# Optimization experiments

Hardware: AMD Instinct MI355X
Metric: run time of the kernel (lower is better)

Reference implementation:

```python
import jax, jax.numpy as jnp
import numpy as np

D_MODEL = 1024
N_HEADS = 16
D_HEAD = 64
B, S = 2, 2048


def setup_inputs() -> dict:
    key = jax.random.key(0)
    ks = jax.random.split(key, 16)
    HDH = N_HEADS * D_HEAD
    s = 0.02
    return {
        "h": jax.random.normal(ks[0], (B, S, D_MODEL), dtype=jnp.float32),
        "att_mask": jax.random.randint(ks[1], (B, S), 0, 2) > 0,
        "Wq": jax.random.normal(ks[2], (D_MODEL, HDH), dtype=jnp.float32) * s,
        "bq": jnp.zeros((HDH,), dtype=jnp.float32),
        "Wkv": jax.random.normal(ks[3], (D_MODEL, 2 * HDH), dtype=jnp.float32) * s,
        "bkv": jnp.zeros((2 * HDH,), dtype=jnp.float32),
        "Wo": jax.random.normal(ks[4], (HDH, D_MODEL), dtype=jnp.float32) * s,
        "bo": jnp.zeros((D_MODEL,), dtype=jnp.float32),
        "W1": jax.random.normal(ks[5], (D_MODEL, D_MODEL), dtype=jnp.float32) * s,
        "b1": jnp.zeros((D_MODEL,), dtype=jnp.float32),
        "W2": jax.random.normal(ks[6], (D_MODEL, D_MODEL), dtype=jnp.float32) * s,
        "b2": jnp.zeros((D_MODEL,), dtype=jnp.float32),
        "ln_g": jnp.ones((D_MODEL,), dtype=jnp.float32),
        "ln_b": jnp.zeros((D_MODEL,), dtype=jnp.float32),
    }


def _layer_norm(x, g, b, eps=1e-6):
    mu = jnp.mean(x, axis=-1, keepdims=True)
    var = jnp.mean(jnp.square(x - mu), axis=-1, keepdims=True)
    return (x - mu) * jax.lax.rsqrt(var + eps) * g + b


def reference(h, att_mask, Wq, bq, Wkv, bkv, Wo, bo, W1, b1, W2, b2, ln_g, ln_b):
    bz, ln, _ = h.shape
    scale = 1.0 / (D_HEAD ** 0.5)
    q = (h @ Wq + bq).reshape(bz, ln, N_HEADS, D_HEAD)
    kv = h @ Wkv + bkv
    k, v = jnp.split(kv, 2, axis=-1)
    k = k.reshape(bz, ln, N_HEADS, D_HEAD)
    v = v.reshape(bz, ln, N_HEADS, D_HEAD)
    # scores: [b, heads, len_q, len_k]
    scores = jnp.einsum('bqhd,bkhd->bhqk', q, k) * scale
    scores = jnp.where(att_mask[:, None, None, :], -1e9, scores)
    probs = jax.nn.softmax(scores, axis=-1)
    att = jnp.einsum('bhqk,bkhd->bqhd', probs, v).reshape(bz, ln, N_HEADS * D_HEAD)
    att_out = att @ Wo + bo
    # glu_type == 1
    g = jax.nn.sigmoid(h @ W1 + b1) * (h @ W2 + b2)
    return _layer_norm(h + att_out + g, ln_g, ln_b)
```

## Files before the change

### kernel.cpp

```cpp
#include <hip/hip_runtime.h>
#include <hip/hip_bf16.h>


typedef short bf16x8 __attribute__((ext_vector_type(8)));
typedef float f32x4  __attribute__((ext_vector_type(4)));
typedef float f32x16 __attribute__((ext_vector_type(16)));
typedef unsigned int u32x4 __attribute__((ext_vector_type(4)));

typedef const __attribute__((address_space(1))) void* gas_cvp;
typedef __attribute__((address_space(3))) void* las_vp;

__device__ __forceinline__ void gload_lds16(const void* g, void* l) {
  __builtin_amdgcn_global_load_lds((gas_cvp)g, (las_vp)l, 16, 0, 0);
}

__device__ __forceinline__ short f2bf(float f) {
  __hip_bfloat16 h = __float2bfloat16(f);
  return *reinterpret_cast<short*>(&h);
}
__device__ __forceinline__ float bf2f(short s) {
  unsigned u = ((unsigned)(unsigned short)s) << 16;
  return __builtin_bit_cast(float, u);
}

#if __has_builtin(__builtin_amdgcn_exp2f)
#define EXP2(x) __builtin_amdgcn_exp2f(x)
#else
#define EXP2(x) exp2f(x)
#endif

constexpr int BATCH = 2;
constexpr int SEQ   = 2048;
constexpr int NH    = 16;
constexpr int MROWS = BATCH * SEQ;
constexpr int NSPLIT = 4;
constexpr int KSPL   = SEQ / NSPLIT;
constexpr int RH     = MROWS * NH;


__global__ __launch_bounds__(256) void cvt_bf16(const float* __restrict__ src,
                                                short* __restrict__ dst, int n4) {
  int i = blockIdx.x * 256 + threadIdx.x;
  if (i >= n4) return;
  float4 v = reinterpret_cast<const float4*>(src)[i];
  short4 o;
  o.x = f2bf(v.x); o.y = f2bf(v.y); o.z = f2bf(v.z); o.w = f2bf(v.w);
  reinterpret_cast<short4*>(dst)[i] = o;
}

struct WtA {
  const float* s[6];
  short* d[6];
  int st[6];
};
__global__ __launch_bounds__(256) void wtrans6(WtA a) {
  __shared__ float tile[32][33];
  const float* __restrict__ src = a.s[blockIdx.z];
  short* __restrict__ dst = a.d[blockIdx.z];
  const int stride = a.st[blockIdx.z];
  const int tx = threadIdx.x & 31, ty = threadIdx.x >> 5;
  const int n0 = blockIdx.x * 32, k0 = blockIdx.y * 32;
  #pragma unroll
  for (int i = 0; i < 32; i += 8)
    tile[ty + i][tx] = src[(size_t)(k0 + ty + i) * stride + n0 + tx];
  __syncthreads();
  #pragma unroll
  for (int i = 0; i < 32; i += 8)
    dst[(size_t)(n0 + ty + i) * 1024 + k0 + tx] = f2bf(tile[tx][ty + i]);
}

__global__ __launch_bounds__(256) void vtrans(const short* __restrict__ qkv,
                                              short* __restrict__ vt) {
  __shared__ short tile[32][33];
  const int tx = threadIdx.x & 31, ty = threadIdx.x >> 5;
  const int s0 = blockIdx.x * 32, d0 = blockIdx.y * 32, b = blockIdx.z;
  #pragma unroll
  for (int i = 0; i < 32; i += 8)
    tile[ty + i][tx] = qkv[(size_t)(b * SEQ + s0 + ty + i) * 3072 + 2048 + d0 + tx];
  __syncthreads();
  #pragma unroll
  for (int i = 0; i < 32; i += 8)
    vt[(size_t)(b * 1024 + d0 + ty + i) * SEQ + s0 + tx] = tile[tx][ty + i];
}

__global__ void pack_bias(const float* __restrict__ bq, const float* __restrict__ bkv,
                          const float* __restrict__ b1, const float* __restrict__ b2,
                          float* __restrict__ bqkv, float* __restrict__ b12) {
  int i = blockIdx.x * 256 + threadIdx.x;
  if (i < 1024) bqkv[i] = bq[i];
  else if (i < 3072) bqkv[i] = bkv[i - 1024];
  else if (i < 4096) b12[i - 3072] = b1[i - 3072];
  else if (i < 5120) b12[i - 3072] = b2[i - 4096];
}

__device__ __forceinline__ bool mask_at(const void* mp, int idx, int flag) {
  if (flag == 1) return ((const int*)mp)[idx] != 0;
  if (flag == 2) return ((const float*)mp)[idx] != 0.f;
  return ((const unsigned char*)mp)[idx] != 0;
}

__global__ __launch_bounds__(256) void premask(const void* __restrict__ msk,
                                               float* __restrict__ mbL) {
  __shared__ int si, sf;
  const unsigned* m = (const unsigned*)msk;
  if (threadIdx.x == 0) { si = 1; sf = 1; }
  __syncthreads();
  bool oki = true, okf = true;
  for (int i = threadIdx.x; i < 1024; i += 256) {
    unsigned v = m[i];
    oki = oki && (v <= 1u);
    okf = okf && (v == 0u || v == 0x3F800000u);
  }
  if (!oki) si = 0;
  if (!okf) sf = 0;
  __syncthreads();
  const int flag = si ? 1 : (sf ? 2 : 0);
  int i = blockIdx.x * 256 + threadIdx.x;
  if (i < MROWS) mbL[i] = mask_at(msk, i, flag) ? -1.442695e9f : -8.0f;
}

__global__ __launch_bounds__(256) void gemm_kernel(const short* __restrict__ A,
                                                   const short* __restrict__ BT,
                                                   const float* __restrict__ bias,
                                                   short* __restrict__ outp, int N) {
  __shared__ short Alds[4096];
  __shared__ short Blds[4096];
  const int tid = threadIdx.x;
  const int w = tid >> 6, lane = tid & 63, g = lane >> 4, lr = lane & 15;
  const int wr = w >> 1, wc = w & 1;
  const int bm = blockIdx.y, bn = blockIdx.x;

  f32x4 acc[4][4] = {};

  const int srow = tid >> 2;
  const int scol = (tid & 3) * 8;
  const short* Ab = A  + (size_t)(bm * 128 + srow) * 1024 + scol;
  const short* Bb = BT + (size_t)(bn * 128 + srow) * 1024 + scol;

  for (int kt = 0; kt < 32; ++kt) {
    const int kb = kt * 32;
    __syncthreads();
    gload_lds16(Ab + kb,             &Alds[tid * 8]);
    gload_lds16(Ab + 64 * 1024 + kb, &Alds[2048 + tid * 8]);
    gload_lds16(Bb + kb,             &Blds[tid * 8]);
    gload_lds16(Bb + 64 * 1024 + kb, &Blds[2048 + tid * 8]);
    asm volatile("s_waitcnt vmcnt(0)" ::: "memory");
    __syncthreads();

    bf16x8 af[4], bfr[4];
    #pragma unroll
    for (int m = 0; m < 4; ++m)
      af[m] = *reinterpret_cast<const bf16x8*>(&Alds[(wr * 64 + m * 16 + lr) * 32 + g * 8]);
    #pragma unroll
    for (int n = 0; n < 4; ++n)
      bfr[n] = *reinterpret_cast<const bf16x8*>(&Blds[(wc * 64 + n * 16 + lr) * 32 + g * 8]);
    #pragma unroll
    for (int m = 0; m < 4; ++m)
      #pragma unroll
      for (int n = 0; n < 4; ++n)
        acc[m][n] = __builtin_amdgcn_mfma_f32_16x16x32_bf16(af[m], bfr[n], acc[m][n], 0, 0, 0);
  }

  #pragma unroll
  for (int m = 0; m < 4; ++m) {
    const int row = bm * 128 + wr * 64 + m * 16 + g * 4;
    #pragma unroll
    for (int n = 0; n < 4; ++n) {
      const int col = bn * 128 + wc * 64 + n * 16 + lr;
      const float bv = bias[col];
      #pragma unroll
      for (int r = 0; r < 4; ++r)
        outp[(size_t)(row + r) * N + col] = f2bf(acc[m][n][r] + bv);
    }
  }
}

__global__ __launch_bounds__(256) void glu_kernel(const short* __restrict__ x12,
                                                  short* __restrict__ g) {
  const int i = blockIdx.x * 256 + threadIdx.x;
  const int row = i >> 7, c8 = (i & 127) * 8;
  const size_t base = (size_t)row * 2048 + c8;
  bf16x8 a = *reinterpret_cast<const bf16x8*>(&x12[base]);
  bf16x8 b = *reinterpret_cast<const bf16x8*>(&x12[base + 1024]);
  bf16x8 r;
  #pragma unroll
  for (int j = 0; j < 8; ++j) {
    const float x = bf2f(a[j]);
    r[j] = f2bf(bf2f(b[j]) / (1.f + __expf(-x)));
  }
  *reinterpret_cast<bf16x8*>(&g[(size_t)row * 1024 + c8]) = r;
}

constexpr int KB = 64;

__global__ __launch_bounds__(256) void attn_kernel(const short* __restrict__ qkv,
                                                   const short* __restrict__ vt,
                                                   const float* __restrict__ mbL,
                                                   short* __restrict__ opart,
                                                   float* __restrict__ spart) {
  __shared__ short Kl[2][64][64];
  __shared__ short Vl[2][64][64];
  __shared__ float mb[KSPL];

  const int tid = threadIdx.x;
  const int w = tid >> 6, lane = tid & 63, ql = lane & 31, hi = lane >> 5;
  const int sp = blockIdx.x & (NSPLIT - 1), qb = blockIdx.x / NSPLIT;
  const int h = blockIdx.y, b = blockIdx.z;
  const int qrow = qb * 128 + w * 32 + ql;
  const int kofs = sp * KSPL;

  bf16x8 qf[4];
  {
    const short* qp = qkv + (size_t)(b * SEQ + qrow) * 3072 + h * 64;
    #pragma unroll
    for (int c = 0; c < 4; ++c)
      qf[c] = *reinterpret_cast<const bf16x8*>(qp + c * 16 + hi * 8);
  }

  const int srow = tid >> 3, sg = tid & 7;
  auto stageKV = [&](int buf, int kt) {
    #pragma unroll
    for (int r = 0; r < 2; ++r) {
      const int row = r * 32 + srow;
      const int gsw = (sg ^ (row & 7)) * 8;
      const short* gk = qkv + (size_t)(b * SEQ + kofs + kt * KB + row) * 3072 + 1024 + h * 64 + gsw;
      gload_lds16(gk, &Kl[buf][0][0] + (r * 256 + tid) * 8);
      const short* gv = vt + (size_t)(b * 1024 + h * 64 + row) * SEQ + kofs + kt * KB + gsw;
      gload_lds16(gv, &Vl[buf][0][0] + (r * 256 + tid) * 8);
    }
  };

  float s_run = 0.f;
  f32x16 oacc0 = {}, oacc1 = {};

  if (tid < 128) gload_lds16(mbL + b * SEQ + kofs + tid * 4, &mb[tid * 4]);
  stageKV(0, 0);
  asm volatile("s_waitcnt vmcnt(0)" ::: "memory");
  __syncthreads();

  constexpr int NT = KSPL / KB;
  for (int kt = 0; kt < NT; ++kt) {
    const int cur = kt & 1;
    if (kt + 1 < NT) stageKV(cur ^ 1, kt + 1);
    const short* Kb = &Kl[cur][0][0];
    const short* Vb = &Vl[cur][0][0];

    #pragma unroll
    for (int t2 = 0; t2 < 2; ++t2) {
      const int krow = t2 * 32 + ql;
      f32x16 sc = {};
      __builtin_amdgcn_s_setprio(1);
      #pragma unroll
      for (int c = 0; c < 4; ++c) {
        bf16x8 kf = *reinterpret_cast<const bf16x8*>(
            Kb + krow * 64 + ((2 * c + hi) ^ (krow & 7)) * 8);
        sc = __builtin_amdgcn_mfma_f32_32x32x16_bf16(kf, qf[c], sc, 0, 0, 0);
      }
      __builtin_amdgcn_s_setprio(0);
      float p[16];
      #pragma unroll
      for (int u = 0; u < 4; ++u) {
        float4 m4 = *reinterpret_cast<const float4*>(&mb[kt * KB + t2 * 32 + u * 8 + hi * 4]);
        p[4 * u + 0] = EXP2(fmaf(sc[4 * u + 0], 0.18033688f, m4.x));
        p[4 * u + 1] = EXP2(fmaf(sc[4 * u + 1], 0.18033688f, m4.y));
        p[4 * u + 2] = EXP2(fmaf(sc[4 * u + 2], 0.18033688f, m4.z));
        p[4 * u + 3] = EXP2(fmaf(sc[4 * u + 3], 0.18033688f, m4.w));
      }
      {
        float a0 = (p[0] + p[1]) + (p[2] + p[3]);
        float a1 = (p[4] + p[5]) + (p[6] + p[7]);
        float a2 = (p[8] + p[9]) + (p[10] + p[11]);
        float a3 = (p[12] + p[13]) + (p[14] + p[15]);
        s_run += (a0 + a1) + (a2 + a3);
      }
      unsigned P[8];
      #pragma unroll
      for (int j = 0; j < 8; ++j)
        asm("v_cvt_pk_bf16_f32 %0, %1, %2" : "=v"(P[j]) : "v"(p[2 * j]), "v"(p[2 * j + 1]));
      asm("v_permlane32_swap_b32 %0, %1" : "+v"(P[0]), "+v"(P[2]));
      asm("v_permlane32_swap_b32 %0, %1" : "+v"(P[1]), "+v"(P[3]));
      asm("v_permlane32_swap_b32 %0, %1" : "+v"(P[4]), "+v"(P[6]));
      asm("v_permlane32_swap_b32 %0, %1" : "+v"(P[5]), "+v"(P[7]));
      u32x4 c0 = { P[0], P[1], P[2], P[3] };
      u32x4 c1 = { P[4], P[5], P[6], P[7] };
      bf16x8 pf[2] = { __builtin_bit_cast(bf16x8, c0), __builtin_bit_cast(bf16x8, c1) };

      __builtin_amdgcn_s_setprio(1);
      #pragma unroll
      for (int ch = 0; ch < 2; ++ch) {
        const int gk = t2 * 4 + ch * 2 + hi;
        bf16x8 v0 = *reinterpret_cast<const bf16x8*>(
            Vb + ql * 64 + (gk ^ (ql & 7)) * 8);
        bf16x8 v1 = *reinterpret_cast<const bf16x8*>(
            Vb + (32 + ql) * 64 + (gk ^ (ql & 7)) * 8);
        oacc0 = __builtin_amdgcn_mfma_f32_32x32x16_bf16(v0, pf[ch], oacc0, 0, 0, 0);
        oacc1 = __builtin_amdgcn_mfma_f32_32x32x16_bf16(v1, pf[ch], oacc1, 0, 0, 0);
      }
      __builtin_amdgcn_s_setprio(0);
    }
    asm volatile("s_waitcnt vmcnt(0)" ::: "memory");
    __syncthreads();
  }

  const float sT = s_run + __shfl_xor(s_run, 32);
  const size_t obase = (size_t)sp * RH * 64 + (size_t)(b * SEQ + qrow) * 1024 + h * 64;
  #pragma unroll
  for (int dt = 0; dt < 2; ++dt) {
    #pragma unroll
    for (int u = 0; u < 4; ++u) {
      short4 st;
      const f32x16& oa = dt ? oacc1 : oacc0;
      st.x = f2bf(oa[4 * u + 0]);
      st.y = f2bf(oa[4 * u + 1]);
      st.z = f2bf(oa[4 * u + 2]);
      st.w = f2bf(oa[4 * u + 3]);
      *reinterpret_cast<short4*>(&opart[obase + dt * 32 + u * 8 + hi * 4]) = st;
    }
  }
  if (hi == 0)
    spart[sp * RH + (b * SEQ + qrow) * NH + h] = sT;
}

__global__ __launch_bounds__(256) void attn_merge(const short* __restrict__ opart,
                                                  const float* __restrict__ spart,
                                                  short* __restrict__ att) {
  const int idx = blockIdx.x * 256 + threadIdx.x;
  const int rh = idx >> 3;
  const size_t base = (size_t)rh * 64 + (idx & 7) * 8;
  float acc[8] = {};
  float ss = 0.f;
  #pragma unroll
  for (int s = 0; s < NSPLIT; ++s) {
    bf16x8 o = *reinterpret_cast<const bf16x8*>(&opart[(size_t)s * RH * 64 + base]);
    #pragma unroll
    for (int j = 0; j < 8; ++j) acc[j] += bf2f(o[j]);
    ss += spart[s * RH + rh];
  }
  const float inv = 1.f / ss;
  bf16x8 r;
  #pragma unroll
  for (int j = 0; j < 8; ++j) r[j] = f2bf(acc[j] * inv);
  *reinterpret_cast<bf16x8*>(&att[base]) = r;
}

__global__ __launch_bounds__(256) void ln_kernel(const float* __restrict__ h,
                                                 const short* __restrict__ ao,
                                                 const short* __restrict__ gl,
                                                 const float* __restrict__ gamma,
                                                 const float* __restrict__ beta,
                                                 float* __restrict__ out) {
  const int row = blockIdx.x;
  const size_t base = (size_t)row * 1024;
  const int t = threadIdx.x;
  __shared__ float red[4];
  float x[4];
  #pragma unroll
  for (int j = 0; j < 4; ++j) {
    const int c = t + j * 256;
    x[j] = h[base + c] + bf2f(ao[base + c]) + bf2f(gl[base + c]);
  }
  float s = x[0] + x[1] + x[2] + x[3];
  #pragma unroll
  for (int d = 1; d < 64; d <<= 1) s += __shfl_xor(s, d);
  if ((t & 63) == 0) red[t >> 6] = s;
  __syncthreads();
  const float mu = (red[0] + red[1] + red[2] + red[3]) * (1.f / 1024.f);
  __syncthreads();
  float vs = 0.f;
  #pragma unroll
  for (int j = 0; j < 4; ++j) { const float dx = x[j] - mu; vs += dx * dx; }
  #pragma unroll
  for (int d = 1; d < 64; d <<= 1) vs += __shfl_xor(vs, d);
  if ((t & 63) == 0) red[t >> 6] = vs;
  __syncthreads();
  const float var = (red[0] + red[1] + red[2] + red[3]) * (1.f / 1024.f);
  const float rs = rsqrtf(var + 1e-6f);
  #pragma unroll
  for (int j = 0; j < 4; ++j) {
    const int c = t + j * 256;
    out[base + c] = (x[j] - mu) * rs * gamma[c] + beta[c];
  }
}


extern "C" void kernel_launch(void* const* d_in, const int* in_sizes, int n_in,
                              void* d_out, int out_size, void* d_ws, size_t ws_size,
                              hipStream_t stream) {
  const float* h   = (const float*)d_in[0];
  const void*  msk = d_in[1];
  const float* Wq  = (const float*)d_in[2];
  const float* bq  = (const float*)d_in[3];
  const float* Wkv = (const float*)d_in[4];
  const float* bkv = (const float*)d_in[5];
  const float* Wo  = (const float*)d_in[6];
  const float* bo  = (const float*)d_in[7];
  const float* W1  = (const float*)d_in[8];
  const float* b1  = (const float*)d_in[9];
  const float* W2  = (const float*)d_in[10];
  const float* b2  = (const float*)d_in[11];
  const float* lng = (const float*)d_in[12];
  const float* lnb = (const float*)d_in[13];
  float* out = (float*)d_out;

  char* ws = (char*)d_ws;
  size_t off = 0;
  auto alloc = [&](size_t bytes) {
    char* p = ws + off;
    off += (bytes + 255) & ~(size_t)255;
    return p;
  };
  short* X     = (short*)alloc((size_t)MROWS * 1024 * 2);
  short* WqkvT = (short*)alloc((size_t)3072 * 1024 * 2);
  short* WoT   = (short*)alloc((size_t)1024 * 1024 * 2);
  short* W1T   = (short*)alloc((size_t)1024 * 1024 * 2);
  short* W2T   = (short*)alloc((size_t)1024 * 1024 * 2);
  float* bqkv  = (float*)alloc(3072 * 4);
  float* b12   = (float*)alloc(2048 * 4);
  float* MBL   = (float*)alloc((size_t)MROWS * 4);
  short* QKV   = (short*)alloc((size_t)MROWS * 3072 * 2);
  short* VT    = (short*)alloc((size_t)BATCH * 1024 * SEQ * 2);
  short* ATT   = (short*)alloc((size_t)MROWS * 1024 * 2);
  short* X1    = (short*)alloc((size_t)MROWS * 1024 * 2);
  short* AO    = (short*)alloc((size_t)MROWS * 1024 * 2);
  short* OP    = (short*)alloc((size_t)NSPLIT * RH * 64 * 2);
  float* SP    = (float*)alloc((size_t)NSPLIT * RH * 4);
  short* X12   = OP;
  if (off > ws_size) return;

  cvt_bf16<<<4096, 256, 0, stream>>>(h, X, MROWS * 1024 / 4);
  WtA wa;
  wa.s[0] = Wq;          wa.d[0] = WqkvT;                wa.st[0] = 1024;
  wa.s[1] = Wkv;         wa.d[1] = WqkvT + 1024 * 1024;  wa.st[1] = 2048;
  wa.s[2] = Wkv + 1024;  wa.d[2] = WqkvT + 2048 * 1024;  wa.st[2] = 2048;
  wa.s[3] = Wo;          wa.d[3] = WoT;                  wa.st[3] = 1024;
  wa.s[4] = W1;          wa.d[4] = W1T;                  wa.st[4] = 1024;
  wa.s[5] = W2;          wa.d[5] = W2T;                  wa.st[5] = 1024;
  wtrans6<<<dim3(32, 32, 6), 256, 0, stream>>>(wa);
  pack_bias<<<20, 256, 0, stream>>>(bq, bkv, b1, b2, bqkv, b12);
  premask<<<16, 256, 0, stream>>>(msk, MBL);

  gemm_kernel<<<dim3(24, 32), 256, 0, stream>>>(X, WqkvT, bqkv, QKV, 3072);
  vtrans<<<dim3(64, 32, 2), 256, 0, stream>>>(QKV, VT);
  attn_kernel<<<dim3(16 * NSPLIT, 16, 2), 256, 0, stream>>>(QKV, VT, MBL, OP, SP);
  attn_merge<<<RH * 8 / 256, 256, 0, stream>>>(OP, SP, ATT);
  gemm_kernel<<<dim3(16, 32), 256, 0, stream>>>(X, W1T, b12, X12, 2048);
  glu_kernel<<<MROWS * 1024 / 8 / 256, 256, 0, stream>>>(X12, X1);
  gemm_kernel<<<dim3(8, 32), 256, 0, stream>>>(ATT, WoT, bo, AO, 1024);
  ln_kernel<<<MROWS, 256, 0, stream>>>(h, AO, X1, lng, lnb, out);
}
```

Baseline: 184.4 us.

## Stage attention K/V tiles through registers with padded LDS and larger key block

The attention kernel now loads 128-key K/V tiles into registers during compute and writes them to a padded LDS layout at the end of each iteration. This replaces direct global-to-LDS loads and XOR swizzling. The padded slots (130 and 65 strides) are meant to avoid bank conflicts with simpler addressing, and doubling KB halves the number of barriers. The cost is more registers for the 8 staged vectors and more LDS, which may lower occupancy.

```diff
diff --git a/kernel.cpp b/kernel.cpp
--- a/kernel.cpp
+++ b/kernel.cpp
@@ -191,15 +191,17 @@
   *reinterpret_cast<bf16x8*>(&g[(size_t)row * 1024 + c8]) = r;
 }
 
-constexpr int KB = 64;
+constexpr int KB = 128;
+constexpr int KSLOT = 8 * 130;
+constexpr int VSLOT = 16 * 65;
 
 __global__ __launch_bounds__(256) void attn_kernel(const short* __restrict__ qkv,
                                                    const short* __restrict__ vt,
                                                    const float* __restrict__ mbL,
                                                    short* __restrict__ opart,
                                                    float* __restrict__ spart) {
-  __shared__ short Kl[2][64][64];
-  __shared__ short Vl[2][64][64];
+  __shared__ short Kl[2][KSLOT * 8];
+  __shared__ short Vl[2][VSLOT * 8];
   __shared__ float mb[KSPL];
 
   const int tid = threadIdx.x;
@@ -217,43 +219,64 @@
       qf[c] = *reinterpret_cast<const bf16x8*>(qp + c * 16 + hi * 8);
   }
 
-  const int srow = tid >> 3, sg = tid & 7;
-  auto stageKV = [&](int buf, int kt) {
-    #pragma unroll
-    for (int r = 0; r < 2; ++r) {
-      const int row = r * 32 + srow;
-      const int gsw = (sg ^ (row & 7)) * 8;
-      const short* gk = qkv + (size_t)(b * SEQ + kofs + kt * KB + row) * 3072 + 1024 + h * 64 + gsw;
-      gload_lds16(gk, &Kl[buf][0][0] + (r * 256 + tid) * 8);
-      const short* gv = vt + (size_t)(b * 1024 + h * 64 + row) * SEQ + kofs + kt * KB + gsw;
-      gload_lds16(gv, &Vl[buf][0][0] + (r * 256 + tid) * 8);
-    }
+  const short* gkbase = qkv + (size_t)(b * SEQ + kofs) * 3072 + 1024 + h * 64
+                        + (size_t)(tid >> 3) * 3072 + (tid & 7) * 8;
+  const short* gvbase = vt + ((size_t)(b * 1024 + h * 64) + (tid >> 4)) * SEQ + kofs
+                        + (tid & 15) * 8;
+  short* kwr0 = &Kl[0][((tid & 7) * 130 + (tid >> 3)) * 8];
+  short* vwr0 = &Vl[0][((tid & 15) * 65 + (tid >> 4)) * 8];
+
+  u32x4 kreg0, kreg1, kreg2, kreg3, vreg0, vreg1, vreg2, vreg3;
+  auto loadTile = [&](int kt) {
+    const short* gk = gkbase + (size_t)kt * KB * 3072;
+    kreg0 = *reinterpret_cast<const u32x4*>(gk);
+    kreg1 = *reinterpret_cast<const u32x4*>(gk + 32 * 3072);
+    kreg2 = *reinterpret_cast<const u32x4*>(gk + 64 * 3072);
+    kreg3 = *reinterpret_cast<const u32x4*>(gk + 96 * 3072);
+    const short* gv = gvbase + kt * KB;
+    vreg0 = *reinterpret_cast<const u32x4*>(gv);
+    vreg1 = *reinterpret_cast<const u32x4*>(gv + 16 * SEQ);
+    vreg2 = *reinterpret_cast<const u32x4*>(gv + 32 * SEQ);
+    vreg3 = *reinterpret_cast<const u32x4*>(gv + 48 * SEQ);
+  };
+  auto writeTile = [&](int buf) {
+    short* kd = kwr0 + buf * KSLOT * 8;
+    *reinterpret_cast<u32x4*>(kd)            = kreg0;
+    *reinterpret_cast<u32x4*>(kd + 32 * 8)   = kreg1;
+    *reinterpret_cast<u32x4*>(kd + 64 * 8)   = kreg2;
+    *reinterpret_cast<u32x4*>(kd + 96 * 8)   = kreg3;
+    short* vd = vwr0 + buf * VSLOT * 8;
+    *reinterpret_cast<u32x4*>(vd)            = vreg0;
+    *reinterpret_cast<u32x4*>(vd + 16 * 8)   = vreg1;
+    *reinterpret_cast<u32x4*>(vd + 32 * 8)   = vreg2;
+    *reinterpret_cast<u32x4*>(vd + 48 * 8)   = vreg3;
   };
 
   float s_run = 0.f;
   f32x16 oacc0 = {}, oacc1 = {};
 
   if (tid < 128) gload_lds16(mbL + b * SEQ + kofs + tid * 4, &mb[tid * 4]);
-  stageKV(0, 0);
-  asm volatile("s_waitcnt vmcnt(0)" ::: "memory");
-  __syncthreads();
+  loadTile(0);
+  writeTile(0);
+  __syncthreads();
+
+  const short* krd0 = &Kl[0][(hi * 130 + ql) * 8];
+  const short* vrd0 = &Vl[0][(hi * 65 + ql) * 8];
 
   constexpr int NT = KSPL / KB;
   for (int kt = 0; kt < NT; ++kt) {
     const int cur = kt & 1;
-    if (kt + 1 < NT) stageKV(cur ^ 1, kt + 1);
-    const short* Kb = &Kl[cur][0][0];
-    const short* Vb = &Vl[cur][0][0];
-
-    #pragma unroll
-    for (int t2 = 0; t2 < 2; ++t2) {
-      const int krow = t2 * 32 + ql;
+    if (kt + 1 < NT) loadTile(kt + 1);
+    const short* Kb = krd0 + cur * KSLOT * 8;
+    const short* Vb = vrd0 + cur * VSLOT * 8;
+
+    #pragma unroll
+    for (int t2 = 0; t2 < 4; ++t2) {
       f32x16 sc = {};
       __builtin_amdgcn_s_setprio(1);
       #pragma unroll
       for (int c = 0; c < 4; ++c) {
-        bf16x8 kf = *reinterpret_cast<const bf16x8*>(
-            Kb + krow * 64 + ((2 * c + hi) ^ (krow & 7)) * 8);
+        bf16x8 kf = *reinterpret_cast<const bf16x8*>(Kb + (c * 260 + t2 * 32) * 8);
         sc = __builtin_amdgcn_mfma_f32_32x32x16_bf16(kf, qf[c], sc, 0, 0, 0);
       }
       __builtin_amdgcn_s_setprio(0);
@@ -288,18 +311,18 @@
       __builtin_amdgcn_s_setprio(1);
       #pragma unroll
       for (int ch = 0; ch < 2; ++ch) {
-        const int gk = t2 * 4 + ch * 2 + hi;
-        bf16x8 v0 = *reinterpret_cast<const bf16x8*>(
-            Vb + ql * 64 + (gk ^ (ql & 7)) * 8);
-        bf16x8 v1 = *reinterpret_cast<const bf16x8*>(
-            Vb + (32 + ql) * 64 + (gk ^ (ql & 7)) * 8);
+        const int gb = (t2 * 4 + ch * 2) * 65;
+        bf16x8 v0 = *reinterpret_cast<const bf16x8*>(Vb + gb * 8);
+        bf16x8 v1 = *reinterpret_cast<const bf16x8*>(Vb + (gb + 32) * 8);
         oacc0 = __builtin_amdgcn_mfma_f32_32x32x16_bf16(v0, pf[ch], oacc0, 0, 0, 0);
         oacc1 = __builtin_amdgcn_mfma_f32_32x32x16_bf16(v1, pf[ch], oacc1, 0, 0, 0);
       }
       __builtin_amdgcn_s_setprio(0);
     }
-    asm volatile("s_waitcnt vmcnt(0)" ::: "memory");
-    __syncthreads();
+    if (kt + 1 < NT) {
+      writeTile(cur ^ 1);
+      __syncthreads();
+    }
   }
 
   const float sT = s_run + __shfl_xor(s_run, 32);
```

After: 186.7 us. No clear change (+1.2%).

## Double-buffer GEMM LDS tiles and restage attention K/V through registers with padding

Applied to the files above, without the earlier changes.

The GEMM kernel now double-buffers its A/B LDS tiles, so the next k-tile's global-to-LDS load is issued before the current tile's MFMAs instead of stalling at the top of each iteration. The attention kernel replaces direct global-to-LDS swizzled double buffers with a single padded LDS buffer filled from registers. Next-tile K/V loads are prefetched into VGPRs during compute and written after a barrier, with a padded slot layout meant to avoid bank conflicts. This trades attention LDS footprint for extra VGPRs and an added barrier per tile, and doubles GEMM LDS usage.

```diff
diff --git a/kernel.cpp b/kernel.cpp
--- a/kernel.cpp
+++ b/kernel.cpp
@@ -123,8 +123,8 @@
                                                    const short* __restrict__ BT,
                                                    const float* __restrict__ bias,
                                                    short* __restrict__ outp, int N) {
-  __shared__ short Alds[4096];
-  __shared__ short Blds[4096];
+  __shared__ short Alds[2][4096];
+  __shared__ short Blds[2][4096];
   const int tid = threadIdx.x;
   const int w = tid >> 6, lane = tid & 63, g = lane >> 4, lr = lane & 15;
   const int wr = w >> 1, wc = w & 1;
@@ -137,28 +137,37 @@
   const short* Ab = A  + (size_t)(bm * 128 + srow) * 1024 + scol;
   const short* Bb = BT + (size_t)(bn * 128 + srow) * 1024 + scol;
 
+  auto stage = [&](int buf, int kt) {
+    const int kb = kt * 32;
+    gload_lds16(Ab + kb,             &Alds[buf][tid * 8]);
+    gload_lds16(Ab + 64 * 1024 + kb, &Alds[buf][2048 + tid * 8]);
+    gload_lds16(Bb + kb,             &Blds[buf][tid * 8]);
+    gload_lds16(Bb + 64 * 1024 + kb, &Blds[buf][2048 + tid * 8]);
+  };
+
+  stage(0, 0);
+  asm volatile("s_waitcnt vmcnt(0)" ::: "memory");
+  __syncthreads();
+
   for (int kt = 0; kt < 32; ++kt) {
-    const int kb = kt * 32;
-    __syncthreads();
-    gload_lds16(Ab + kb,             &Alds[tid * 8]);
-    gload_lds16(Ab + 64 * 1024 + kb, &Alds[2048 + tid * 8]);
-    gload_lds16(Bb + kb,             &Blds[tid * 8]);
-    gload_lds16(Bb + 64 * 1024 + kb, &Blds[2048 + tid * 8]);
+    const int cur = kt & 1;
+    if (kt + 1 < 32) stage(cur ^ 1, kt + 1);
+
+    bf16x8 af[4], bfr[4];
+    #pragma unroll
+    for (int m = 0; m < 4; ++m)
+      af[m] = *reinterpret_cast<const bf16x8*>(&Alds[cur][(wr * 64 + m * 16 + lr) * 32 + g * 8]);
+    #pragma unroll
+    for (int n = 0; n < 4; ++n)
+      bfr[n] = *reinterpret_cast<const bf16x8*>(&Blds[cur][(wc * 64 + n * 16 + lr) * 32 + g * 8]);
+    #pragma unroll
+    for (int m = 0; m < 4; ++m)
+      #pragma unroll
+      for (int n = 0; n < 4; ++n)
+        acc[m][n] = __builtin_amdgcn_mfma_f32_16x16x32_bf16(af[m], bfr[n], acc[m][n], 0, 0, 0);
+
     asm volatile("s_waitcnt vmcnt(0)" ::: "memory");
     __syncthreads();
-
-    bf16x8 af[4], bfr[4];
-    #pragma unroll
-    for (int m = 0; m < 4; ++m)
-      af[m] = *reinterpret_cast<const bf16x8*>(&Alds[(wr * 64 + m * 16 + lr) * 32 + g * 8]);
-    #pragma unroll
-    for (int n = 0; n < 4; ++n)
-      bfr[n] = *reinterpret_cast<const bf16x8*>(&Blds[(wc * 64 + n * 16 + lr) * 32 + g * 8]);
-    #pragma unroll
-    for (int m = 0; m < 4; ++m)
-      #pragma unroll
-      for (int n = 0; n < 4; ++n)
-        acc[m][n] = __builtin_amdgcn_mfma_f32_16x16x32_bf16(af[m], bfr[n], acc[m][n], 0, 0, 0);
   }
 
   #pragma unroll
@@ -192,14 +201,16 @@
 }
 
 constexpr int KB = 64;
+constexpr int KSLOT = 8 * 66;
+constexpr int VSLOT = 8 * 66;
 
 __global__ __launch_bounds__(256) void attn_kernel(const short* __restrict__ qkv,
                                                    const short* __restrict__ vt,
                                                    const float* __restrict__ mbL,
                                                    short* __restrict__ opart,
                                                    float* __restrict__ spart) {
-  __shared__ short Kl[2][64][64];
-  __shared__ short Vl[2][64][64];
+  __shared__ short Kl[KSLOT * 8];
+  __shared__ short Vl[VSLOT * 8];
   __shared__ float mb[KSPL];
 
   const int tid = threadIdx.x;
@@ -217,43 +228,51 @@
       qf[c] = *reinterpret_cast<const bf16x8*>(qp + c * 16 + hi * 8);
   }
 
-  const int srow = tid >> 3, sg = tid & 7;
-  auto stageKV = [&](int buf, int kt) {
-    #pragma unroll
-    for (int r = 0; r < 2; ++r) {
-      const int row = r * 32 + srow;
-      const int gsw = (sg ^ (row & 7)) * 8;
-      const short* gk = qkv + (size_t)(b * SEQ + kofs + kt * KB + row) * 3072 + 1024 + h * 64 + gsw;
-      gload_lds16(gk, &Kl[buf][0][0] + (r * 256 + tid) * 8);
-      const short* gv = vt + (size_t)(b * 1024 + h * 64 + row) * SEQ + kofs + kt * KB + gsw;
-      gload_lds16(gv, &Vl[buf][0][0] + (r * 256 + tid) * 8);
-    }
+  const short* gkbase = qkv + (size_t)(b * SEQ + kofs) * 3072 + 1024 + h * 64
+                        + (size_t)(tid >> 3) * 3072 + (tid & 7) * 8;
+  const short* gvbase = vt + ((size_t)(b * 1024 + h * 64) + (tid >> 3)) * SEQ + kofs
+                        + (tid & 7) * 8;
+  short* kwr = &Kl[((tid & 7) * 66 + (tid >> 3)) * 8];
+  short* vwr = &Vl[((tid & 7) * 66 + (tid >> 3)) * 8];
+
+  u32x4 kreg0, kreg1, vreg0, vreg1;
+  auto loadTile = [&](int kt) {
+    const short* gk = gkbase + (size_t)kt * KB * 3072;
+    kreg0 = *reinterpret_cast<const u32x4*>(gk);
+    kreg1 = *reinterpret_cast<const u32x4*>(gk + 32 * 3072);
+    const short* gv = gvbase + kt * KB;
+    vreg0 = *reinterpret_cast<const u32x4*>(gv);
+    vreg1 = *reinterpret_cast<const u32x4*>(gv + 32 * SEQ);
+  };
+  auto writeTile = [&]() {
+    *reinterpret_cast<u32x4*>(kwr)          = kreg0;
+    *reinterpret_cast<u32x4*>(kwr + 32 * 8) = kreg1;
+    *reinterpret_cast<u32x4*>(vwr)          = vreg0;
+    *reinterpret_cast<u32x4*>(vwr + 32 * 8) = vreg1;
   };
 
   float s_run = 0.f;
   f32x16 oacc0 = {}, oacc1 = {};
 
   if (tid < 128) gload_lds16(mbL + b * SEQ + kofs + tid * 4, &mb[tid * 4]);
-  stageKV(0, 0);
-  asm volatile("s_waitcnt vmcnt(0)" ::: "memory");
-  __syncthreads();
+  loadTile(0);
+  writeTile();
+  __syncthreads();
+
+  const short* krd = &Kl[(hi * 66 + ql) * 8];
+  const short* vrd = &Vl[(hi * 66 + ql) * 8];
 
   constexpr int NT = KSPL / KB;
   for (int kt = 0; kt < NT; ++kt) {
-    const int cur = kt & 1;
-    if (kt + 1 < NT) stageKV(cur ^ 1, kt + 1);
-    const short* Kb = &Kl[cur][0][0];
-    const short* Vb = &Vl[cur][0][0];
+    if (kt + 1 < NT) loadTile(kt + 1);
 
     #pragma unroll
     for (int t2 = 0; t2 < 2; ++t2) {
-      const int krow = t2 * 32 + ql;
       f32x16 sc = {};
       __builtin_amdgcn_s_setprio(1);
       #pragma unroll
       for (int c = 0; c < 4; ++c) {
-        bf16x8 kf = *reinterpret_cast<const bf16x8*>(
-            Kb + krow * 64 + ((2 * c + hi) ^ (krow & 7)) * 8);
+        bf16x8 kf = *reinterpret_cast<const bf16x8*>(krd + (c * 132 + t2 * 32) * 8);
         sc = __builtin_amdgcn_mfma_f32_32x32x16_bf16(kf, qf[c], sc, 0, 0, 0);
       }
       __builtin_amdgcn_s_setprio(0);
@@ -288,18 +307,20 @@
       __builtin_amdgcn_s_setprio(1);
       #pragma unroll
       for (int ch = 0; ch < 2; ++ch) {
-        const int gk = t2 * 4 + ch * 2 + hi;
-        bf16x8 v0 = *reinterpret_cast<const bf16x8*>(
-            Vb + ql * 64 + (gk ^ (ql & 7)) * 8);
-        bf16x8 v1 = *reinterpret_cast<const bf16x8*>(
-            Vb + (32 + ql) * 64 + (gk ^ (ql & 7)) * 8);
+        const int gb = (t2 * 4 + ch * 2) * 66;
+        bf16x8 v0 = *reinterpret_cast<const bf16x8*>(vrd + gb * 8);
+        bf16x8 v1 = *reinterpret_cast<const bf16x8*>(vrd + (gb + 32) * 8);
         oacc0 = __builtin_amdgcn_mfma_f32_32x32x16_bf16(v0, pf[ch], oacc0, 0, 0, 0);
         oacc1 = __builtin_amdgcn_mfma_f32_32x32x16_bf16(v1, pf[ch], oacc1, 0, 0, 0);
       }
       __builtin_amdgcn_s_setprio(0);
     }
-    asm volatile("s_waitcnt vmcnt(0)" ::: "memory");
-    __syncthreads();
+
+    if (kt + 1 < NT) {
+      __syncthreads();
+      writeTile();
+      __syncthreads();
+    }
   }
 
   const float sT = s_run + __shfl_xor(s_run, 32);
```

Result: slower. 193.4 us (+4.9%).
